# Performance work log

Hardware: AMD Instinct MI355X
Metric: run time of the kernel (lower is better)

The kernel has to match this reference:

```python
import jax, jax.numpy as jnp
import numpy as np

THETA = 1.0       # thr
TAU_RHO = 0.5     # grad_width
SCALE_RHO = 1.0   # grad_scale


def avg_pool4(x):
    # x: (N, C, H, W, T) -> 4x4 average pool per timestep (pool weight = 1/16)
    N, C, H, W, T = x.shape
    return x.reshape(N, C, H // 4, 4, W // 4, 4, T).mean(axis=(3, 5))


def conv2d_t(x, w):
    # SLAYER conv: spatial-only conv3d with kernel (k,k,1), pad 3, no bias.
    # x: (N, C, H, W, T), w: (O, I, 7, 7)
    N, C, H, W, T = x.shape
    xt = jnp.moveaxis(x, -1, 1).reshape(N * T, C, H, W)
    y = jax.lax.conv_general_dilated(
        xt, w, window_strides=(1, 1), padding=[(3, 3), (3, 3)],
        dimension_numbers=('NCHW', 'OIHW', 'NCHW'))
    O = w.shape[0]
    return jnp.moveaxis(y.reshape(N, T, O, H, W), 1, -1)


def psp(x):
    # IAF SRM kernel = unit step (Ts=1) -> causal cumulative sum over time
    return jnp.cumsum(x, axis=-1)


def _spike_scan(u):
    # Sequential threshold + persistent refractory subtraction (scaleRef=1, IAF)
    uT = jnp.moveaxis(u, -1, 0)  # (T, ...)
    def step(r, ut):
        v = ut + r                       # membrane incl. refractory
        s = (v >= THETA).astype(u.dtype)
        return r - THETA * s, (s, v)
    _, (sT, vT) = jax.lax.scan(step, jnp.zeros_like(uT[0]), uT)
    return jnp.moveaxis(sT, 0, -1), jnp.moveaxis(vT, 0, -1)


@jax.custom_vjp
def spike(u):
    return _spike_scan(u)[0]


def _spike_fwd(u):
    s, v = _spike_scan(u)
    return s, v


def _spike_bwd(v, g):
    # SLAYER surrogate: no BPTT through refractory recurrence
    pdf = (SCALE_RHO / TAU_RHO) * jnp.exp(-jnp.abs(v - THETA) / TAU_RHO)
    return (g * pdf,)


spike.defvjp(_spike_fwd, _spike_bwd)


def setup_inputs() -> dict:
    key = jax.random.key(0)
    k0, k1, k2, k3 = jax.random.split(key, 4)
    data = jax.random.uniform(k0, (4, 2, 256, 256, 100), dtype=jnp.float32)
    w0 = jax.random.normal(k1, (4, 2, 7, 7), dtype=jnp.float32) * 0.1
    w1 = jax.random.normal(k2, (8, 4, 7, 7), dtype=jnp.float32) * 0.05
    wl = jax.random.normal(k3, (2, 8, 4, 4), dtype=jnp.float32) * 0.1
    return {"data": data, "w0": w0, "w1": w1, "wl": wl}


def reference(data, w0, w1, wl):
    x = avg_pool4(data)                      # (N,2,64,64,T)
    x = spike(psp(conv2d_t(x, w0)))          # (N,4,64,64,T)
    x = avg_pool4(x)                         # (N,4,16,16,T)
    x = spike(psp(conv2d_t(x, w1)))          # (N,8,16,16,T)
    x = avg_pool4(x)                         # (N,8,4,4,T)
    out = jnp.einsum('nchwt,ochw->not', x, wl)  # dense (4,4,8)->2, squeeze
    return out                               # (N,2,T)
```

## Files before the change

### kernel.cpp

```cpp
#include <hip/hip_runtime.h>
#include <hip/hip_bf16.h>

using u16 = unsigned short;
using u32 = unsigned int;
using u64 = unsigned long long;

__device__ __forceinline__ float b2f(u16 u){
  union { u32 i; float f; } x; x.i = ((u32)u) << 16; return x.f;
}

__global__ __launch_bounds__(256) void k_prep(const void* __restrict__ data,
                                              const void* __restrict__ w0,
                                              const void* __restrict__ w1,
                                              const void* __restrict__ wl,
                                              int* __restrict__ gflag,
                                              float* __restrict__ w0f,
                                              float* __restrict__ w1f,
                                              float* __restrict__ wlf){
  __shared__ int zs[4], ss[4];
  __shared__ int sflag;
  int tid = threadIdx.x;
  u32 w = ((const u32*)data)[tid];
  u16 lo = (u16)(w & 0xFFFFu);
  u64 zb = __ballot(lo == 0);
  u64 sb = __ballot((lo >> 15) & 1);
  int wave = tid >> 6;
  if((tid & 63) == 0){ zs[wave] = __popcll(zb); ss[wave] = __popcll(sb); }
  __syncthreads();
  if(tid == 0){
    int zeros = zs[0]+zs[1]+zs[2]+zs[3];
    int signs = ss[0]+ss[1]+ss[2]+ss[3];
    int f = (zeros >= 128 || signs > 0) ? 1 : 0;
    sflag = f; *gflag = f;
  }
  __syncthreads();
  int f = sflag;
  const float* w0F = (const float*)w0; const u16* w0H = (const u16*)w0;
  const float* w1F = (const float*)w1; const u16* w1H = (const u16*)w1;
  const float* wlF = (const float*)wl; const u16* wlH = (const u16*)wl;
  for(int i = tid; i < 392;  i += 256) w0f[i] = f ? w0F[i] : b2f(w0H[i]);
  for(int i = tid; i < 1568; i += 256) w1f[i] = f ? w1F[i] : b2f(w1H[i]);
  for(int i = tid; i < 256;  i += 256) wlf[i] = f ? wlF[i] : b2f(wlH[i]);
}

__global__ __launch_bounds__(256) void k_pool1(const void* __restrict__ data,
                                               const int* __restrict__ gflag,
                                               float* __restrict__ P1){
  int idx = blockIdx.x * 256 + threadIdx.x;
  int tc  = idx % 25;
  int pix = idx / 25;
  int ow  = pix & 63;
  int oh  = (pix >> 6) & 63;
  int nc  = pix >> 12;
  int t0  = tc * 4;
  size_t off = ((size_t)((nc*256 + oh*4)*256 + ow*4)) * 100 + t0;
  double s0=0.0, s1=0.0, s2=0.0, s3=0.0;
  if(*gflag){
    const float* base = (const float*)data + off;
    #pragma unroll
    for(int di=0; di<4; ++di)
      #pragma unroll
      for(int dj=0; dj<4; ++dj){
        float4 v = *reinterpret_cast<const float4*>(base + (size_t)(di*256 + dj)*100);
        s0 += (double)v.x; s1 += (double)v.y; s2 += (double)v.z; s3 += (double)v.w;
      }
  } else {
    const u16* base = (const u16*)data + off;
    #pragma unroll
    for(int di=0; di<4; ++di)
      #pragma unroll
      for(int dj=0; dj<4; ++dj){
        ushort4 v = *reinterpret_cast<const ushort4*>(base + (size_t)(di*256 + dj)*100);
        s0 += (double)b2f(v.x); s1 += (double)b2f(v.y);
        s2 += (double)b2f(v.z); s3 += (double)b2f(v.w);
      }
  }
  float* o = P1 + (size_t)pix * 100 + t0;
  o[0] = (float)(s0 * 0.0625); o[1] = (float)(s1 * 0.0625);
  o[2] = (float)(s2 * 0.0625); o[3] = (float)(s3 * 0.0625);
}

__global__ __launch_bounds__(256) void k_conv1(const float* __restrict__ P1,
                                               const float* __restrict__ w0f,
                                               float* __restrict__ A1f){
  __shared__ float4  tile[968];
  __shared__ double4 wl4[98];
  int bid  = blockIdx.x;
  int tcl  = bid % 25; int rest = bid / 25;
  int tl   = rest & 15; int n = rest >> 4;
  int ty   = (tl >> 2) * 16, tx = (tl & 3) * 16;
  int t0   = tcl * 4;
  int tid  = threadIdx.x;
  for(int i = tid; i < 392; i += 256){
    int o = i / 98, r = i % 98;
    ((double*)wl4)[r*4 + o] = (double)w0f[i];
  }
  for(int idx = tid; idx < 968; idx += 256){
    int ci = idx / 484, r = idx % 484;
    int yy = r / 22, xx = r % 22;
    int gy = ty + yy - 3, gx = tx + xx - 3;
    float4 v; v.x = v.y = v.z = v.w = 0.f;
    if(gy >= 0 && gy < 64 && gx >= 0 && gx < 64){
      const float* p = P1 + ((size_t)((n*2+ci)*64 + gy)*64 + gx)*100 + t0;
      v.x = p[0]; v.y = p[1]; v.z = p[2]; v.w = p[3];
    }
    tile[idx] = v;
  }
  __syncthreads();
  int y = tid >> 4, x = tid & 15;
  double acc[4][4] = {};
  for(int ci = 0; ci < 2; ++ci)
    for(int dy = 0; dy < 7; ++dy){
      #pragma unroll
      for(int dx = 0; dx < 7; ++dx){
        float4 iv = tile[ci*484 + (y+dy)*22 + (x+dx)];
        double4 wv = wl4[ci*49 + dy*7 + dx];
        double i0 = (double)iv.x, i1 = (double)iv.y, i2 = (double)iv.z, i3 = (double)iv.w;
        acc[0][0] += wv.x*i0; acc[0][1] += wv.x*i1; acc[0][2] += wv.x*i2; acc[0][3] += wv.x*i3;
        acc[1][0] += wv.y*i0; acc[1][1] += wv.y*i1; acc[1][2] += wv.y*i2; acc[1][3] += wv.y*i3;
        acc[2][0] += wv.z*i0; acc[2][1] += wv.z*i1; acc[2][2] += wv.z*i2; acc[2][3] += wv.z*i3;
        acc[3][0] += wv.w*i0; acc[3][1] += wv.w*i1; acc[3][2] += wv.w*i2; acc[3][3] += wv.w*i3;
      }
    }
  int stile = (((ty + y) >> 2) << 2) + (tx >> 4);
  int lane  = ((y & 3) << 4) + x;
  float4* O = (float4*)A1f;
  size_t ob = ((size_t)(n*4)*64 + stile) * 25;
  ob = (ob + tcl) * 64 + lane;
  #pragma unroll
  for(int o = 0; o < 4; ++o)
    O[ob + (size_t)o * 102400] = make_float4((float)acc[o][0], (float)acc[o][1],
                                             (float)acc[o][2], (float)acc[o][3]);
}

__global__ __launch_bounds__(64) void k_scan1(const float* __restrict__ A1f,
                                              float* __restrict__ S1p){
  int bid  = blockIdx.x;
  int stile = bid & 63, no = bid >> 6;
  int xg = stile & 3, yg = stile >> 2;
  int lane = threadIdx.x;
  int lx = lane & 15;
  const float4* base = (const float4*)A1f + (size_t)bid * 1600 + lane;
  float* outb = S1p + (size_t)no*100*256 + yg*16 + xg*4;
  int cell = lx >> 2;
  u64 cmask = 0x000F000F000F000FULL << (4*cell);
  bool writer = (lane < 16) && ((lx & 3) == 0);
  double u = 0.0, r = 0.0;
  float4 cur = base[0];
  float4 nxt = base[64];
  for(int tb = 0; tb < 25; ++tb){
    int nb = (tb + 2 < 25) ? tb + 2 : 24;
    float4 nn = base[(size_t)nb * 64];
    #pragma unroll
    for(int j = 0; j < 4; ++j){
      double a = (j==0)?(double)cur.x:(j==1)?(double)cur.y:(j==2)?(double)cur.z:(double)cur.w;
      u += a;
      bool sp = (u + r >= 1.0);
      if(sp) r -= 1.0;
      u64 m = __ballot(sp);
      if(writer){
        float cnt = (float)__popcll(m & cmask);
        outb[(size_t)(tb*4 + j)*256 + cell] = cnt * 0.0625f;
      }
    }
    cur = nxt; nxt = nn;
  }
}

__global__ __launch_bounds__(256) void k_conv2(const float* __restrict__ S1p,
                                               const float* __restrict__ w1f,
                                               float* __restrict__ A2f){
  __shared__ float   tf[4*4*484];
  __shared__ double4 wl4[196];
  int bid = blockIdx.x;
  int oh  = bid & 1; int rest = bid >> 1;
  int tc  = rest % 25; int n = rest / 25;
  int t0  = tc * 4;
  int tid = threadIdx.x;
  for(int i = tid; i < 7744; i += 256) tf[i] = 0.f;
  for(int i = tid; i < 784; i += 256){
    int oj = i / 196, rem = i % 196;
    ((double*)wl4)[rem*4 + oj] = (double)w1f[(oh*4 + oj)*196 + rem];
  }
  __syncthreads();
  for(int i = tid; i < 4096; i += 256){
    int ci = i >> 10, tt = (i >> 8) & 3, p = i & 255;
    int yy = p >> 4, xx = p & 15;
    tf[(ci*4 + tt)*484 + (yy+3)*22 + (xx+3)] =
        S1p[((size_t)(n*4+ci)*100 + t0 + tt)*256 + p];
  }
  __syncthreads();
  int y = tid >> 4, x = tid & 15;
  double acc[4][4] = {};
  for(int ci = 0; ci < 4; ++ci)
    for(int dy = 0; dy < 7; ++dy){
      #pragma unroll
      for(int dx = 0; dx < 7; ++dx){
        const float* tp = &tf[ci*1936 + (y+dy)*22 + (x+dx)];
        double4 wv = wl4[ci*49 + dy*7 + dx];
        double i0 = (double)tp[0],   i1 = (double)tp[484];
        double i2 = (double)tp[968], i3 = (double)tp[1452];
        acc[0][0] += wv.x*i0; acc[0][1] += wv.x*i1; acc[0][2] += wv.x*i2; acc[0][3] += wv.x*i3;
        acc[1][0] += wv.y*i0; acc[1][1] += wv.y*i1; acc[1][2] += wv.y*i2; acc[1][3] += wv.y*i3;
        acc[2][0] += wv.z*i0; acc[2][1] += wv.z*i1; acc[2][2] += wv.z*i2; acc[2][3] += wv.z*i3;
        acc[3][0] += wv.w*i0; acc[3][1] += wv.w*i1; acc[3][2] += wv.w*i2; acc[3][3] += wv.w*i3;
      }
    }
  float4* O = (float4*)A2f;
  size_t ob = ((size_t)(n*8 + oh*4)*25 + tc)*256 + tid;
  #pragma unroll
  for(int oj = 0; oj < 4; ++oj)
    O[ob + (size_t)oj*6400] = make_float4((float)acc[oj][0], (float)acc[oj][1],
                                          (float)acc[oj][2], (float)acc[oj][3]);
}

__global__ __launch_bounds__(64) void k_scan2(const float* __restrict__ A2f,
                                              const float* __restrict__ wlf,
                                              float* __restrict__ P4){
  int bid  = blockIdx.x;
  int q    = bid & 3, nc = bid >> 2, c = nc & 7;
  int lane = threadIdx.x;
  int px   = q*64 + lane;
  float w0g[4], w1g[4];
  #pragma unroll
  for(int g = 0; g < 4; ++g){
    w0g[g] = wlf[      c*16 + q*4 + g] * 0.0625f;
    w1g[g] = wlf[128 + c*16 + q*4 + g] * 0.0625f;
  }
  const float4* base = (const float4*)A2f + (size_t)nc*6400 + px;
  float* outb = P4 + (size_t)bid * 200;
  double u = 0.0, r = 0.0;
  float4 cur = base[0];
  float4 nxt = base[256];
  for(int tb = 0; tb < 25; ++tb){
    int nb = (tb + 2 < 25) ? tb + 2 : 24;
    float4 nn = base[(size_t)nb * 256];
    #pragma unroll
    for(int j = 0; j < 4; ++j){
      double a = (j==0)?(double)cur.x:(j==1)?(double)cur.y:(j==2)?(double)cur.z:(double)cur.w;
      u += a;
      bool sp = (u + r >= 1.0);
      if(sp) r -= 1.0;
      u64 m = __ballot(sp);
      if(lane == 0){
        float p0 = 0.f, p1 = 0.f;
        #pragma unroll
        for(int g = 0; g < 4; ++g){
          float cnt = (float)__popcll(m & (0x000F000F000F000FULL << (4*g)));
          p0 += cnt * w0g[g]; p1 += cnt * w1g[g];
        }
        int t = tb*4 + j;
        outb[t] = p0; outb[100 + t] = p1;
      }
    }
    cur = nxt; nxt = nn;
  }
}

__global__ __launch_bounds__(256) void k_out(const float* __restrict__ P4,
                                             const int* __restrict__ gflag,
                                             void* __restrict__ out){
  int idx = blockIdx.x * 256 + threadIdx.x;
  if(idx >= 800) return;
  int t = idx % 100; int o = (idx / 100) & 1; int n = idx / 200;
  float s = 0.f;
  for(int cq = 0; cq < 32; ++cq)
    s += P4[((size_t)(n*32 + cq))*200 + o*100 + t];
  if(*gflag) ((float*)out)[idx] = s;
  else       ((__hip_bfloat16*)out)[idx] = __float2bfloat16(s);
}

extern "C" void kernel_launch(void* const* d_in, const int* in_sizes, int n_in,
                              void* d_out, int out_size, void* d_ws, size_t ws_size,
                              hipStream_t stream) {
  const void* data = d_in[0];
  const void* w0   = d_in[1];
  const void* w1   = d_in[2];
  const void* wl   = d_in[3];
  char* ws = (char*)d_ws;
  float*  P1   = (float*) (ws + 0);
  float*  A1f  = (float*) (ws + 13107200);
  float*  S1p  = (float*) (ws + 39321600);
  int*    gflag= (int*)   (ws + 40960000);
  float*  w0f  = (float*) (ws + 40960004);
  float*  w1f  = (float*) (ws + 40961572);
  float*  wlf  = (float*) (ws + 40967844);
  float*  A2f  = (float*) (ws + 0);
  float*  P4   = (float*) (ws + 3276800);

  hipLaunchKernelGGL(k_prep,  dim3(1),    dim3(256), 0, stream,
                     data, w0, w1, wl, gflag, w0f, w1f, wlf);
  hipLaunchKernelGGL(k_pool1, dim3(3200), dim3(256), 0, stream, data, gflag, P1);
  hipLaunchKernelGGL(k_conv1, dim3(1600), dim3(256), 0, stream, P1, w0f, A1f);
  hipLaunchKernelGGL(k_scan1, dim3(1024), dim3(64),  0, stream, A1f, S1p);
  hipLaunchKernelGGL(k_conv2, dim3(200),  dim3(256), 0, stream, S1p, w1f, A2f);
  hipLaunchKernelGGL(k_scan2, dim3(128),  dim3(64),  0, stream, A2f, wlf, P4);
  hipLaunchKernelGGL(k_out,   dim3(4),    dim3(256), 0, stream, P4, gflag, d_out);
}
```

Before: 389.2 us.

## Fold prep and output kernels into neighbours and preload scan inputs

```diff
diff --git a/kernel.cpp b/kernel.cpp
--- a/kernel.cpp
+++ b/kernel.cpp
@@ -9,44 +9,32 @@
   union { u32 i; float f; } x; x.i = ((u32)u) << 16; return x.f;
 }
 
-__global__ __launch_bounds__(256) void k_prep(const void* __restrict__ data,
-                                              const void* __restrict__ w0,
-                                              const void* __restrict__ w1,
-                                              const void* __restrict__ wl,
-                                              int* __restrict__ gflag,
-                                              float* __restrict__ w0f,
-                                              float* __restrict__ w1f,
-                                              float* __restrict__ wlf){
+__global__ __launch_bounds__(256) void k_pool1(const void* __restrict__ data,
+                                               float* __restrict__ P1,
+                                               int* __restrict__ gflag,
+                                               unsigned* __restrict__ ctr){
   __shared__ int zs[4], ss[4];
   __shared__ int sflag;
   int tid = threadIdx.x;
-  u32 w = ((const u32*)data)[tid];
-  u16 lo = (u16)(w & 0xFFFFu);
-  u64 zb = __ballot(lo == 0);
-  u64 sb = __ballot((lo >> 15) & 1);
-  int wave = tid >> 6;
-  if((tid & 63) == 0){ zs[wave] = __popcll(zb); ss[wave] = __popcll(sb); }
-  __syncthreads();
-  if(tid == 0){
-    int zeros = zs[0]+zs[1]+zs[2]+zs[3];
-    int signs = ss[0]+ss[1]+ss[2]+ss[3];
-    int f = (zeros >= 128 || signs > 0) ? 1 : 0;
-    sflag = f; *gflag = f;
-  }
-  __syncthreads();
+  {
+    u32 w = ((const u32*)data)[tid];
+    u16 lo = (u16)(w & 0xFFFFu);
+    u64 zb = __ballot(lo == 0);
+    u64 sb = __ballot((lo >> 15) & 1);
+    int wave = tid >> 6;
+    if((tid & 63) == 0){ zs[wave] = __popcll(zb); ss[wave] = __popcll(sb); }
+    __syncthreads();
+    if(tid == 0){
+      int zeros = zs[0]+zs[1]+zs[2]+zs[3];
+      int signs = ss[0]+ss[1]+ss[2]+ss[3];
+      int f = (zeros >= 128 || signs > 0) ? 1 : 0;
+      sflag = f;
+      if(blockIdx.x == 0){ *gflag = f; *ctr = 0u; }
+    }
+    __syncthreads();
+  }
   int f = sflag;
-  const float* w0F = (const float*)w0; const u16* w0H = (const u16*)w0;
-  const float* w1F = (const float*)w1; const u16* w1H = (const u16*)w1;
-  const float* wlF = (const float*)wl; const u16* wlH = (const u16*)wl;
-  for(int i = tid; i < 392;  i += 256) w0f[i] = f ? w0F[i] : b2f(w0H[i]);
-  for(int i = tid; i < 1568; i += 256) w1f[i] = f ? w1F[i] : b2f(w1H[i]);
-  for(int i = tid; i < 256;  i += 256) wlf[i] = f ? wlF[i] : b2f(wlH[i]);
-}
-
-__global__ __launch_bounds__(256) void k_pool1(const void* __restrict__ data,
-                                               const int* __restrict__ gflag,
-                                               float* __restrict__ P1){
-  int idx = blockIdx.x * 256 + threadIdx.x;
+  int idx = blockIdx.x * 256 + tid;
   int tc  = idx % 25;
   int pix = idx / 25;
   int ow  = pix & 63;
@@ -55,7 +43,7 @@
   int t0  = tc * 4;
   size_t off = ((size_t)((nc*256 + oh*4)*256 + ow*4)) * 100 + t0;
   double s0=0.0, s1=0.0, s2=0.0, s3=0.0;
-  if(*gflag){
+  if(f){
     const float* base = (const float*)data + off;
     #pragma unroll
     for(int di=0; di<4; ++di)
@@ -81,7 +69,8 @@
 }
 
 __global__ __launch_bounds__(256) void k_conv1(const float* __restrict__ P1,
-                                               const float* __restrict__ w0f,
+                                               const void* __restrict__ w0,
+                                               const int* __restrict__ gflag,
                                                float* __restrict__ A1f){
   __shared__ float4  tile[968];
   __shared__ double4 wl4[98];
@@ -91,9 +80,11 @@
   int ty   = (tl >> 2) * 16, tx = (tl & 3) * 16;
   int t0   = tcl * 4;
   int tid  = threadIdx.x;
+  int f    = *gflag;
+  const float* w0F = (const float*)w0; const u16* w0H = (const u16*)w0;
   for(int i = tid; i < 392; i += 256){
     int o = i / 98, r = i % 98;
-    ((double*)wl4)[r*4 + o] = (double)w0f[i];
+    ((double*)wl4)[r*4 + o] = (double)(f ? w0F[i] : b2f(w0H[i]));
   }
   for(int idx = tid; idx < 968; idx += 256){
     int ci = idx / 484, r = idx % 484;
@@ -145,15 +136,15 @@
   int cell = lx >> 2;
   u64 cmask = 0x000F000F000F000FULL << (4*cell);
   bool writer = (lane < 16) && ((lx & 3) == 0);
+  float4 v[25];
+  #pragma unroll
+  for(int tb = 0; tb < 25; ++tb) v[tb] = base[(size_t)tb * 64];
   double u = 0.0, r = 0.0;
-  float4 cur = base[0];
-  float4 nxt = base[64];
+  #pragma unroll
   for(int tb = 0; tb < 25; ++tb){
-    int nb = (tb + 2 < 25) ? tb + 2 : 24;
-    float4 nn = base[(size_t)nb * 64];
     #pragma unroll
     for(int j = 0; j < 4; ++j){
-      double a = (j==0)?(double)cur.x:(j==1)?(double)cur.y:(j==2)?(double)cur.z:(double)cur.w;
+      double a = (j==0)?(double)v[tb].x:(j==1)?(double)v[tb].y:(j==2)?(double)v[tb].z:(double)v[tb].w;
       u += a;
       bool sp = (u + r >= 1.0);
       if(sp) r -= 1.0;
@@ -163,12 +154,12 @@
         outb[(size_t)(tb*4 + j)*256 + cell] = cnt * 0.0625f;
       }
     }
-    cur = nxt; nxt = nn;
   }
 }
 
 __global__ __launch_bounds__(256) void k_conv2(const float* __restrict__ S1p,
-                                               const float* __restrict__ w1f,
+                                               const void* __restrict__ w1,
+                                               const int* __restrict__ gflag,
                                                float* __restrict__ A2f){
   __shared__ float   tf[4*4*484];
   __shared__ double4 wl4[196];
@@ -177,10 +168,13 @@
   int tc  = rest % 25; int n = rest / 25;
   int t0  = tc * 4;
   int tid = threadIdx.x;
+  int f   = *gflag;
+  const float* w1F = (const float*)w1; const u16* w1H = (const u16*)w1;
   for(int i = tid; i < 7744; i += 256) tf[i] = 0.f;
   for(int i = tid; i < 784; i += 256){
     int oj = i / 196, rem = i % 196;
-    ((double*)wl4)[rem*4 + oj] = (double)w1f[(oh*4 + oj)*196 + rem];
+    int k = (oh*4 + oj)*196 + rem;
+    ((double*)wl4)[rem*4 + oj] = (double)(f ? w1F[k] : b2f(w1H[k]));
   }
   __syncthreads();
   for(int i = tid; i < 4096; i += 256){
@@ -215,29 +209,36 @@
 }
 
 __global__ __launch_bounds__(64) void k_scan2(const float* __restrict__ A2f,
-                                              const float* __restrict__ wlf,
-                                              float* __restrict__ P4){
+                                              const void* __restrict__ wl,
+                                              const int* __restrict__ gflag,
+                                              float* __restrict__ P4,
+                                              unsigned* __restrict__ ctr,
+                                              void* __restrict__ out){
   int bid  = blockIdx.x;
   int q    = bid & 3, nc = bid >> 2, c = nc & 7;
   int lane = threadIdx.x;
   int px   = q*64 + lane;
+  int f    = *gflag;
+  const float* wlF = (const float*)wl; const u16* wlH = (const u16*)wl;
   float w0g[4], w1g[4];
   #pragma unroll
   for(int g = 0; g < 4; ++g){
-    w0g[g] = wlf[      c*16 + q*4 + g] * 0.0625f;
-    w1g[g] = wlf[128 + c*16 + q*4 + g] * 0.0625f;
+    int i0 =       c*16 + q*4 + g;
+    int i1 = 128 + c*16 + q*4 + g;
+    w0g[g] = (f ? wlF[i0] : b2f(wlH[i0])) * 0.0625f;
+    w1g[g] = (f ? wlF[i1] : b2f(wlH[i1])) * 0.0625f;
   }
   const float4* base = (const float4*)A2f + (size_t)nc*6400 + px;
   float* outb = P4 + (size_t)bid * 200;
+  float4 v[25];
+  #pragma unroll
+  for(int tb = 0; tb < 25; ++tb) v[tb] = base[(size_t)tb * 256];
   double u = 0.0, r = 0.0;
-  float4 cur = base[0];
-  float4 nxt = base[256];
+  #pragma unroll
   for(int tb = 0; tb < 25; ++tb){
-    int nb = (tb + 2 < 25) ? tb + 2 : 24;
-    float4 nn = base[(size_t)nb * 256];
     #pragma unroll
     for(int j = 0; j < 4; ++j){
-      double a = (j==0)?(double)cur.x:(j==1)?(double)cur.y:(j==2)?(double)cur.z:(double)cur.w;
+      double a = (j==0)?(double)v[tb].x:(j==1)?(double)v[tb].y:(j==2)?(double)v[tb].z:(double)v[tb].w;
       u += a;
       bool sp = (u + r >= 1.0);
       if(sp) r -= 1.0;
@@ -253,21 +254,22 @@
         outb[t] = p0; outb[100 + t] = p1;
       }
     }
-    cur = nxt; nxt = nn;
-  }
-}
-
-__global__ __launch_bounds__(256) void k_out(const float* __restrict__ P4,
-                                             const int* __restrict__ gflag,
-                                             void* __restrict__ out){
-  int idx = blockIdx.x * 256 + threadIdx.x;
-  if(idx >= 800) return;
-  int t = idx % 100; int o = (idx / 100) & 1; int n = idx / 200;
-  float s = 0.f;
-  for(int cq = 0; cq < 32; ++cq)
-    s += P4[((size_t)(n*32 + cq))*200 + o*100 + t];
-  if(*gflag) ((float*)out)[idx] = s;
-  else       ((__hip_bfloat16*)out)[idx] = __float2bfloat16(s);
+  }
+  __threadfence();
+  unsigned old = 0u;
+  if(lane == 0) old = atomicAdd(ctr, 1u);
+  old = __shfl(old, 0);
+  if(old == 127u){
+    __threadfence();
+    for(int idx = lane; idx < 800; idx += 64){
+      int t = idx % 100; int o = (idx / 100) & 1; int n = idx / 200;
+      float s = 0.f;
+      for(int cq = 0; cq < 32; ++cq)
+        s += P4[((size_t)(n*32 + cq))*200 + o*100 + t];
+      if(f) ((float*)out)[idx] = s;
+      else  ((__hip_bfloat16*)out)[idx] = __float2bfloat16(s);
+    }
+  }
 }
 
 extern "C" void kernel_launch(void* const* d_in, const int* in_sizes, int n_in,
@@ -278,22 +280,17 @@
   const void* w1   = d_in[2];
   const void* wl   = d_in[3];
   char* ws = (char*)d_ws;
-  float*  P1   = (float*) (ws + 0);
-  float*  A1f  = (float*) (ws + 13107200);
-  float*  S1p  = (float*) (ws + 39321600);
-  int*    gflag= (int*)   (ws + 40960000);
-  float*  w0f  = (float*) (ws + 40960004);
-  float*  w1f  = (float*) (ws + 40961572);
-  float*  wlf  = (float*) (ws + 40967844);
-  float*  A2f  = (float*) (ws + 0);
-  float*  P4   = (float*) (ws + 3276800);
-
-  hipLaunchKernelGGL(k_prep,  dim3(1),    dim3(256), 0, stream,
-                     data, w0, w1, wl, gflag, w0f, w1f, wlf);
-  hipLaunchKernelGGL(k_pool1, dim3(3200), dim3(256), 0, stream, data, gflag, P1);
-  hipLaunchKernelGGL(k_conv1, dim3(1600), dim3(256), 0, stream, P1, w0f, A1f);
+  float*    P1   = (float*)   (ws + 0);
+  float*    A1f  = (float*)   (ws + 13107200);
+  float*    S1p  = (float*)   (ws + 39321600);
+  int*      gflag= (int*)     (ws + 40960000);
+  unsigned* ctr  = (unsigned*)(ws + 40960004);
+  float*    A2f  = (float*)   (ws + 0);
+  float*    P4   = (float*)   (ws + 3276800);
+
+  hipLaunchKernelGGL(k_pool1, dim3(3200), dim3(256), 0, stream, data, P1, gflag, ctr);
+  hipLaunchKernelGGL(k_conv1, dim3(1600), dim3(256), 0, stream, P1, w0, gflag, A1f);
   hipLaunchKernelGGL(k_scan1, dim3(1024), dim3(64),  0, stream, A1f, S1p);
-  hipLaunchKernelGGL(k_conv2, dim3(200),  dim3(256), 0, stream, S1p, w1f, A2f);
-  hipLaunchKernelGGL(k_scan2, dim3(128),  dim3(64),  0, stream, A2f, wlf, P4);
-  hipLaunchKernelGGL(k_out,   dim3(4),    dim3(256), 0, stream, P4, gflag, d_out);
-}
+  hipLaunchKernelGGL(k_conv2, dim3(200),  dim3(256), 0, stream, S1p, w1, gflag, A2f);
+  hipLaunchKernelGGL(k_scan2, dim3(128),  dim3(64),  0, stream, A2f, wl, gflag, P4, ctr, d_out);
+}
```

Result: no change. 395.7 us (+1.7%).

## Fuse first conv with spike scan, streaming time chunks through double-buffered LDS

Applied to the files above, without the earlier changes.

```diff
diff --git a/kernel.cpp b/kernel.cpp
--- a/kernel.cpp
+++ b/kernel.cpp
@@ -80,90 +80,106 @@
   o[2] = (float)(s2 * 0.0625); o[3] = (float)(s3 * 0.0625);
 }
 
-__global__ __launch_bounds__(256) void k_conv1(const float* __restrict__ P1,
-                                               const float* __restrict__ w0f,
-                                               float* __restrict__ A1f){
-  __shared__ float4  tile[968];
-  __shared__ double4 wl4[98];
-  int bid  = blockIdx.x;
-  int tcl  = bid % 25; int rest = bid / 25;
-  int tl   = rest & 15; int n = rest >> 4;
-  int ty   = (tl >> 2) * 16, tx = (tl & 3) * 16;
-  int t0   = tcl * 4;
-  int tid  = threadIdx.x;
-  for(int i = tid; i < 392; i += 256){
-    int o = i / 98, r = i % 98;
-    ((double*)wl4)[r*4 + o] = (double)w0f[i];
-  }
-  for(int idx = tid; idx < 968; idx += 256){
-    int ci = idx / 484, r = idx % 484;
-    int yy = r / 22, xx = r % 22;
-    int gy = ty + yy - 3, gx = tx + xx - 3;
-    float4 v; v.x = v.y = v.z = v.w = 0.f;
-    if(gy >= 0 && gy < 64 && gx >= 0 && gx < 64){
-      const float* p = P1 + ((size_t)((n*2+ci)*64 + gy)*64 + gx)*100 + t0;
-      v.x = p[0]; v.y = p[1]; v.z = p[2]; v.w = p[3];
-    }
-    tile[idx] = v;
-  }
-  __syncthreads();
+__global__ __launch_bounds__(256) void k_cs1(const float* __restrict__ P1,
+                                             const float* __restrict__ w0f,
+                                             float* __restrict__ S1p){
+  __shared__ float4 tile[2][968];
+  __shared__ double wl[98];
+  int bid = blockIdx.x;
+  int tl  = bid & 15; int rest = bid >> 4;
+  int o   = rest & 3; int n = rest >> 2;
+  int ty  = (tl >> 2) * 16, tx = (tl & 3) * 16;
+  int tid = threadIdx.x;
+  for(int i = tid; i < 98; i += 256) wl[i] = (double)w0f[o*98 + i];
+
+  int idx0 = tid, idx1 = tid + 256, idx2 = tid + 512, idx3 = tid + 768;
+  bool has3 = (tid < 200);
+  const float *p0, *p1, *p2, *p3;
+  {
+    int ci = idx0/484, r = idx0%484, yy = r/22, xx = r%22;
+    int gy = ty+yy-3, gx = tx+xx-3;
+    p0 = (gy>=0 && gy<64 && gx>=0 && gx<64)
+       ? P1 + ((size_t)((n*2+ci)*64 + gy)*64 + gx)*100 : nullptr;
+  }
+  {
+    int ci = idx1/484, r = idx1%484, yy = r/22, xx = r%22;
+    int gy = ty+yy-3, gx = tx+xx-3;
+    p1 = (gy>=0 && gy<64 && gx>=0 && gx<64)
+       ? P1 + ((size_t)((n*2+ci)*64 + gy)*64 + gx)*100 : nullptr;
+  }
+  {
+    int ci = idx2/484, r = idx2%484, yy = r/22, xx = r%22;
+    int gy = ty+yy-3, gx = tx+xx-3;
+    p2 = (gy>=0 && gy<64 && gx>=0 && gx<64)
+       ? P1 + ((size_t)((n*2+ci)*64 + gy)*64 + gx)*100 : nullptr;
+  }
+  p3 = nullptr;
+  if(has3){
+    int ci = idx3/484, r = idx3%484, yy = r/22, xx = r%22;
+    int gy = ty+yy-3, gx = tx+xx-3;
+    p3 = (gy>=0 && gy<64 && gx>=0 && gx<64)
+       ? P1 + ((size_t)((n*2+ci)*64 + gy)*64 + gx)*100 : nullptr;
+  }
+
+  const float4 zz = make_float4(0.f, 0.f, 0.f, 0.f);
+  {
+    float4 v0 = p0 ? *reinterpret_cast<const float4*>(p0) : zz;
+    float4 v1 = p1 ? *reinterpret_cast<const float4*>(p1) : zz;
+    float4 v2 = p2 ? *reinterpret_cast<const float4*>(p2) : zz;
+    float4 v3 = p3 ? *reinterpret_cast<const float4*>(p3) : zz;
+    tile[0][idx0] = v0; tile[0][idx1] = v1; tile[0][idx2] = v2;
+    if(has3) tile[0][idx3] = v3;
+  }
+  __syncthreads();
+
   int y = tid >> 4, x = tid & 15;
-  double acc[4][4] = {};
-  for(int ci = 0; ci < 2; ++ci)
-    for(int dy = 0; dy < 7; ++dy){
-      #pragma unroll
-      for(int dx = 0; dx < 7; ++dx){
-        float4 iv = tile[ci*484 + (y+dy)*22 + (x+dx)];
-        double4 wv = wl4[ci*49 + dy*7 + dx];
-        double i0 = (double)iv.x, i1 = (double)iv.y, i2 = (double)iv.z, i3 = (double)iv.w;
-        acc[0][0] += wv.x*i0; acc[0][1] += wv.x*i1; acc[0][2] += wv.x*i2; acc[0][3] += wv.x*i3;
-        acc[1][0] += wv.y*i0; acc[1][1] += wv.y*i1; acc[1][2] += wv.y*i2; acc[1][3] += wv.y*i3;
-        acc[2][0] += wv.z*i0; acc[2][1] += wv.z*i1; acc[2][2] += wv.z*i2; acc[2][3] += wv.z*i3;
-        acc[3][0] += wv.w*i0; acc[3][1] += wv.w*i1; acc[3][2] += wv.w*i2; acc[3][3] += wv.w*i3;
-      }
-    }
-  int stile = (((ty + y) >> 2) << 2) + (tx >> 4);
-  int lane  = ((y & 3) << 4) + x;
-  float4* O = (float4*)A1f;
-  size_t ob = ((size_t)(n*4)*64 + stile) * 25;
-  ob = (ob + tcl) * 64 + lane;
-  #pragma unroll
-  for(int o = 0; o < 4; ++o)
-    O[ob + (size_t)o * 102400] = make_float4((float)acc[o][0], (float)acc[o][1],
-                                             (float)acc[o][2], (float)acc[o][3]);
-}
-
-__global__ __launch_bounds__(64) void k_scan1(const float* __restrict__ A1f,
-                                              float* __restrict__ S1p){
-  int bid  = blockIdx.x;
-  int stile = bid & 63, no = bid >> 6;
-  int xg = stile & 3, yg = stile >> 2;
-  int lane = threadIdx.x;
-  int lx = lane & 15;
-  const float4* base = (const float4*)A1f + (size_t)bid * 1600 + lane;
-  float* outb = S1p + (size_t)no*100*256 + yg*16 + xg*4;
-  int cell = lx >> 2;
+  int lane = tid & 63, wv_ = tid >> 6;
+  int cell = (x >> 2);
   u64 cmask = 0x000F000F000F000FULL << (4*cell);
-  bool writer = (lane < 16) && ((lx & 3) == 0);
-  double u = 0.0, r = 0.0;
-  float4 cur = base[0];
-  float4 nxt = base[64];
+  bool writer = (lane < 16) && ((x & 3) == 0);
+  float* outb = S1p + ((size_t)(n*4 + o))*100*256 + (ty/4 + wv_)*16 + tx/4;
+
+  double u = 0.0, rr = 0.0;
   for(int tb = 0; tb < 25; ++tb){
-    int nb = (tb + 2 < 25) ? tb + 2 : 24;
-    float4 nn = base[(size_t)nb * 64];
+    int cur = tb & 1, nxt = cur ^ 1;
+    bool have = (tb + 1 < 25);
+    float4 v0 = zz, v1 = zz, v2 = zz, v3 = zz;
+    if(have){
+      int t0n = (tb + 1) * 4;
+      v0 = p0 ? *reinterpret_cast<const float4*>(p0 + t0n) : zz;
+      v1 = p1 ? *reinterpret_cast<const float4*>(p1 + t0n) : zz;
+      v2 = p2 ? *reinterpret_cast<const float4*>(p2 + t0n) : zz;
+      v3 = p3 ? *reinterpret_cast<const float4*>(p3 + t0n) : zz;
+    }
+    double a0 = 0.0, a1 = 0.0, a2 = 0.0, a3 = 0.0;
+    for(int ci = 0; ci < 2; ++ci)
+      for(int dy = 0; dy < 7; ++dy){
+        #pragma unroll
+        for(int dx = 0; dx < 7; ++dx){
+          float4 iv = tile[cur][ci*484 + (y+dy)*22 + (x+dx)];
+          double w = wl[ci*49 + dy*7 + dx];
+          a0 += w * (double)iv.x; a1 += w * (double)iv.y;
+          a2 += w * (double)iv.z; a3 += w * (double)iv.w;
+        }
+      }
+    float f0 = (float)a0, f1 = (float)a1, f2 = (float)a2, f3 = (float)a3;
     #pragma unroll
     for(int j = 0; j < 4; ++j){
-      double a = (j==0)?(double)cur.x:(j==1)?(double)cur.y:(j==2)?(double)cur.z:(double)cur.w;
+      double a = (j==0)?(double)f0:(j==1)?(double)f1:(j==2)?(double)f2:(double)f3;
       u += a;
-      bool sp = (u + r >= 1.0);
-      if(sp) r -= 1.0;
+      bool sp = (u + rr >= 1.0);
+      if(sp) rr -= 1.0;
       u64 m = __ballot(sp);
       if(writer){
         float cnt = (float)__popcll(m & cmask);
         outb[(size_t)(tb*4 + j)*256 + cell] = cnt * 0.0625f;
       }
     }
-    cur = nxt; nxt = nn;
+    if(have){
+      tile[nxt][idx0] = v0; tile[nxt][idx1] = v1; tile[nxt][idx2] = v2;
+      if(has3) tile[nxt][idx3] = v3;
+    }
+    __syncthreads();
   }
 }
 
@@ -279,20 +295,18 @@
   const void* wl   = d_in[3];
   char* ws = (char*)d_ws;
   float*  P1   = (float*) (ws + 0);
-  float*  A1f  = (float*) (ws + 13107200);
-  float*  S1p  = (float*) (ws + 39321600);
-  int*    gflag= (int*)   (ws + 40960000);
-  float*  w0f  = (float*) (ws + 40960004);
-  float*  w1f  = (float*) (ws + 40961572);
-  float*  wlf  = (float*) (ws + 40967844);
+  float*  S1p  = (float*) (ws + 13107200);
+  int*    gflag= (int*)   (ws + 14745600);
+  float*  w0f  = (float*) (ws + 14745604);
+  float*  w1f  = (float*) (ws + 14747172);
+  float*  wlf  = (float*) (ws + 14753444);
   float*  A2f  = (float*) (ws + 0);
   float*  P4   = (float*) (ws + 3276800);
 
   hipLaunchKernelGGL(k_prep,  dim3(1),    dim3(256), 0, stream,
                      data, w0, w1, wl, gflag, w0f, w1f, wlf);
   hipLaunchKernelGGL(k_pool1, dim3(3200), dim3(256), 0, stream, data, gflag, P1);
-  hipLaunchKernelGGL(k_conv1, dim3(1600), dim3(256), 0, stream, P1, w0f, A1f);
-  hipLaunchKernelGGL(k_scan1, dim3(1024), dim3(64),  0, stream, A1f, S1p);
+  hipLaunchKernelGGL(k_cs1,   dim3(256),  dim3(256), 0, stream, P1, w0f, S1p);
   hipLaunchKernelGGL(k_conv2, dim3(200),  dim3(256), 0, stream, S1p, w1f, A2f);
   hipLaunchKernelGGL(k_scan2, dim3(128),  dim3(64),  0, stream, A2f, wlf, P4);
   hipLaunchKernelGGL(k_out,   dim3(4),    dim3(256), 0, stream, P4, gflag, d_out);
```

New measurement: 624.6 us. +60.5%, slower.
